# Kernel tuning notes

Hardware: AMD Instinct MI355X
Metric: run time of the kernel (lower is better)

## Reference

```python
import jax, jax.numpy as jnp
import numpy as np

HIDDEN = 32
INPUT = 1


def setup_inputs() -> dict:
    key = jax.random.key(0)
    ks = jax.random.split(key, 8)
    B, T = 4096, 512
    s = 1.0 / np.sqrt(HIDDEN)
    return {
        "x": jax.random.normal(ks[0], (B, T, INPUT), dtype=jnp.float32),
        "h0": jnp.zeros((1, B, HIDDEN), dtype=jnp.float32),
        "W_ih": jax.random.uniform(ks[1], (HIDDEN, INPUT), jnp.float32, -s, s),
        "b_ih": jax.random.uniform(ks[2], (HIDDEN,), jnp.float32, -s, s),
        "W_hh": jax.random.uniform(ks[3], (HIDDEN, HIDDEN), jnp.float32, -s, s),
        "b_hh": jax.random.uniform(ks[4], (HIDDEN,), jnp.float32, -s, s),
        "W_out": jax.random.uniform(ks[5], (1, HIDDEN), jnp.float32, -s, s),
        "b_out": jax.random.uniform(ks[6], (1,), jnp.float32, -s, s),
    }


def reference(x, h0, W_ih, b_ih, W_hh, b_hh, W_out, b_out):
    # Precompute input projection for all timesteps: [B, T, H]
    xp = jnp.einsum("bti,hi->bth", x, W_ih) + b_ih

    def step(h, xt):  # h: [B,H], xt: [B,H]
        h_new = jnp.tanh(xt + h @ W_hh.T + b_hh)
        return h_new, h_new

    hT, r_out = jax.lax.scan(step, h0[0], jnp.swapaxes(xp, 0, 1))  # r_out: [T,B,H]
    r_out = jnp.swapaxes(r_out, 0, 1)  # [B,T,H]
    # Per-timestep Linear(32->1) fused into one batched matmul
    outs = jnp.einsum("bth,oh->bto", r_out, W_out) + b_out  # [B,T,1]
    return outs, hT[None]  # h_state: [1,B,H]
```

## Files before the change

### kernel.cpp

```cpp
#include <hip/hip_runtime.h>

#define BATCH 4096
#define SEQT  512
#define HID   32

typedef _Float16 f16;
typedef _Float16 h2 __attribute__((ext_vector_type(2)));

#if __has_builtin(__builtin_amdgcn_fdot2)
#define FDOT2(a, b, c) __builtin_amdgcn_fdot2((a), (b), (c), false)
#else
#define FDOT2(a, b, c) fmaf((float)(a)[1], (float)(b)[1], fmaf((float)(a)[0], (float)(b)[0], (c)))
#endif

#if __has_builtin(__builtin_amdgcn_exp2f)
#define FAST_EXP2(x) __builtin_amdgcn_exp2f(x)
#else
#define FAST_EXP2(x) exp2f(x)
#endif
#if __has_builtin(__builtin_amdgcn_rcpf)
#define FAST_RCP(x) __builtin_amdgcn_rcpf(x)
#else
#define FAST_RCP(x) (1.0f / (x))
#endif

#define DPP_X1  0xB1
#define DPP_X2  0x4E
#define DPP_X7  0x141
#define DPP_X15 0x140

#if __has_builtin(__builtin_amdgcn_update_dpp)
template <int C, typename T>
__device__ __forceinline__ T xl(T v) {
    return __builtin_bit_cast(T, __builtin_amdgcn_update_dpp(
        0, __builtin_bit_cast(int, v), C, 0xF, 0xF, false));
}
#else
template <int C, typename T>
__device__ __forceinline__ T xl(T v) {
    constexpr int m = (C == DPP_X1) ? 1 : (C == DPP_X2) ? 2 : (C == DPP_X7) ? 7 : 15;
    return __builtin_bit_cast(T, __shfl_xor(__builtin_bit_cast(int, v), m));
}
#endif

__global__ __launch_bounds__(256) void rnn_kernel(
    const float* __restrict__ x,
    const float* __restrict__ h0,
    const float* __restrict__ W_ih,
    const float* __restrict__ b_ih,
    const float* __restrict__ W_hh,
    const float* __restrict__ b_hh,
    const float* __restrict__ W_out,
    const float* __restrict__ b_out,
    float* __restrict__ out)
{
    const int tid  = threadIdx.x;
    const int ell  = tid & 15;
    const int bseq = (blockIdx.x * 256 + tid) >> 4;
    const int j0 = 2 * ell, j1 = 2 * ell + 1;

    constexpr int MTBL[16] = {0, 1, 2, 3, 7, 6, 5, 4, 15, 14, 13, 12, 8, 9, 10, 11};

    h2 W0[16], W1[16];
    #pragma unroll
    for (int r = 0; r < 16; ++r) {
        const int p = ell ^ MTBL[r];
        const float2 w0 = *reinterpret_cast<const float2*>(W_hh + j0 * HID + 2 * p);
        const float2 w1 = *reinterpret_cast<const float2*>(W_hh + j1 * HID + 2 * p);
        W0[r] = h2{(f16)w0.x, (f16)w0.y};
        W1[r] = h2{(f16)w1.x, (f16)w1.y};
    }
    const float2 wo = *reinterpret_cast<const float2*>(W_out + j0);
    const h2 Wo2 = h2{(f16)wo.x, (f16)wo.y};
    const float wih0 = W_ih[j0], wih1 = W_ih[j1];
    const float bia0 = b_ih[j0] + b_hh[j0];
    const float bia1 = b_ih[j1] + b_hh[j1];
    const float bout = b_out[0];

    const float2 h0v = *reinterpret_cast<const float2*>(h0 + (size_t)bseq * HID + j0);
    h2 hcur = h2{(f16)h0v.x, (f16)h0v.y};
    float hn0 = h0v.x, hn1 = h0v.y;

    const float* xg = x + (size_t)bseq * SEQT;
    float*       og = out + (size_t)bseq * SEQT;

#define STEP(T2, XC) do {                                                     \
    h2 v0 = hcur;                                                             \
    h2 v1 = xl<DPP_X1>(v0);                                                   \
    h2 v2 = xl<DPP_X2>(v0);                                                   \
    h2 v3 = xl<DPP_X2>(v1);                                                   \
    h2 v4 = xl<DPP_X7>(v0);                                                   \
    h2 v5 = xl<DPP_X7>(v1);                                                   \
    h2 v6 = xl<DPP_X7>(v2);                                                   \
    h2 v7 = xl<DPP_X7>(v3);                                                   \
    h2 v8  = xl<DPP_X15>(v0);                                                 \
    h2 v9  = xl<DPP_X15>(v1);                                                 \
    h2 v10 = xl<DPP_X15>(v2);                                                 \
    h2 v11 = xl<DPP_X15>(v3);                                                 \
    h2 v12 = xl<DPP_X15>(v4);                                                 \
    h2 v13 = xl<DPP_X15>(v5);                                                 \
    h2 v14 = xl<DPP_X15>(v6);                                                 \
    h2 v15 = xl<DPP_X15>(v7);                                                 \
    float a0 = fmaf((XC), wih0, bia0);                                        \
    float b0 = fmaf((XC), wih1, bia1);                                        \
    a0 = FDOT2(v0,  W0[0],  a0);                                              \
    float a1 = FDOT2(v1,  W0[1],  0.0f);                                      \
    float a2 = FDOT2(v2,  W0[2],  0.0f);                                      \
    float a3 = FDOT2(v3,  W0[3],  0.0f);                                      \
    a0 = FDOT2(v4,  W0[4],  a0); a1 = FDOT2(v5,  W0[5],  a1);                 \
    a2 = FDOT2(v6,  W0[6],  a2); a3 = FDOT2(v7,  W0[7],  a3);                 \
    a0 = FDOT2(v8,  W0[8],  a0); a1 = FDOT2(v9,  W0[9],  a1);                 \
    a2 = FDOT2(v10, W0[10], a2); a3 = FDOT2(v11, W0[11], a3);                 \
    a0 = FDOT2(v12, W0[12], a0); a1 = FDOT2(v13, W0[13], a1);                 \
    a2 = FDOT2(v14, W0[14], a2); a3 = FDOT2(v15, W0[15], a3);                 \
    b0 = FDOT2(v0,  W1[0],  b0);                                              \
    float b1 = FDOT2(v1,  W1[1],  0.0f);                                      \
    float b2 = FDOT2(v2,  W1[2],  0.0f);                                      \
    float b3 = FDOT2(v3,  W1[3],  0.0f);                                      \
    b0 = FDOT2(v4,  W1[4],  b0); b1 = FDOT2(v5,  W1[5],  b1);                 \
    b2 = FDOT2(v6,  W1[6],  b2); b3 = FDOT2(v7,  W1[7],  b3);                 \
    b0 = FDOT2(v8,  W1[8],  b0); b1 = FDOT2(v9,  W1[9],  b1);                 \
    b2 = FDOT2(v10, W1[10], b2); b3 = FDOT2(v11, W1[11], b3);                 \
    b0 = FDOT2(v12, W1[12], b0); b1 = FDOT2(v13, W1[13], b1);                 \
    b2 = FDOT2(v14, W1[14], b2); b3 = FDOT2(v15, W1[15], b3);                 \
    const float s0 = (a0 + a1) + (a2 + a3);                                   \
    const float s1 = (b0 + b1) + (b2 + b3);                                   \
    const float e0 = FAST_EXP2(s0 * 2.8853900817779268f);                     \
    const float e1 = FAST_EXP2(s1 * 2.8853900817779268f);                     \
    hn0 = fmaf(-2.0f, FAST_RCP(e0 + 1.0f), 1.0f);                             \
    hn1 = fmaf(-2.0f, FAST_RCP(e1 + 1.0f), 1.0f);                             \
    hcur = h2{(f16)hn0, (f16)hn1};                                            \
    float pp = FDOT2(hcur, Wo2, 0.0f);                                        \
    pp += xl<DPP_X1>(pp);                                                     \
    pp += xl<DPP_X2>(pp);                                                     \
    pp += xl<DPP_X7>(pp);                                                     \
    pp += xl<DPP_X15>(pp);                                                    \
    if (ell == (T2)) osel = pp;                                               \
} while (0)

#define HALF(HC, Q0, Q1, Q2, Q3) do {                                         \
    float osel = 0.0f;                                                        \
    STEP(0,  (Q0).x); STEP(1,  (Q0).y); STEP(2,  (Q0).z); STEP(3,  (Q0).w);   \
    STEP(4,  (Q1).x); STEP(5,  (Q1).y); STEP(6,  (Q1).z); STEP(7,  (Q1).w);   \
    STEP(8,  (Q2).x); STEP(9,  (Q2).y); STEP(10, (Q2).z); STEP(11, (Q2).w);   \
    STEP(12, (Q3).x); STEP(13, (Q3).y); STEP(14, (Q3).z); STEP(15, (Q3).w);   \
    og[(HC) * 16 + ell] = osel + bout;                                        \
} while (0)

    const float4* xq0 = reinterpret_cast<const float4*>(xg);
    float4 qA0 = xq0[0], qA1 = xq0[1], qA2 = xq0[2], qA3 = xq0[3];
    float4 qB0, qB1, qB2, qB3;

    #pragma unroll 1
    for (int hc = 0; hc < 32; hc += 2) {
        const float4* pB = reinterpret_cast<const float4*>(xg + (hc + 1) * 16);
        qB0 = pB[0]; qB1 = pB[1]; qB2 = pB[2]; qB3 = pB[3];
        HALF(hc, qA0, qA1, qA2, qA3);
        const int tn = (hc + 2 < 32) ? (hc + 2) : 0;
        const float4* pA = reinterpret_cast<const float4*>(xg + tn * 16);
        qA0 = pA[0]; qA1 = pA[1]; qA2 = pA[2]; qA3 = pA[3];
        HALF(hc + 1, qB0, qB1, qB2, qB3);
    }

    float2 ht; ht.x = hn0; ht.y = hn1;
    *reinterpret_cast<float2*>(out + (size_t)BATCH * SEQT + (size_t)bseq * HID + j0) = ht;

#undef HALF
#undef STEP
}

extern "C" void kernel_launch(void* const* d_in, const int* in_sizes, int n_in,
                              void* d_out, int out_size, void* d_ws, size_t ws_size,
                              hipStream_t stream) {
    const float* x     = (const float*)d_in[0];
    const float* h0    = (const float*)d_in[1];
    const float* W_ih  = (const float*)d_in[2];
    const float* b_ih  = (const float*)d_in[3];
    const float* W_hh  = (const float*)d_in[4];
    const float* b_hh  = (const float*)d_in[5];
    const float* W_out = (const float*)d_in[6];
    const float* b_out = (const float*)d_in[7];
    float* outp = (float*)d_out;

    dim3 grid(BATCH * 16 / 256);
    dim3 block(256);
    hipLaunchKernelGGL(rnn_kernel, grid, block, 0, stream,
                       x, h0, W_ih, b_ih, W_hh, b_hh, W_out, b_out, outp);
}
```

Before: 168.6 us.

## Switch recurrence to fp32 packed FMA and batch output projection via LDS

Replaces the fp16 fdot2 recurrence with fp32 packed-FMA arithmetic on float2 vectors, which doubles the DPP lane exchanges per step (two 32-bit moves per shuffle). The per-step Linear(32->1) output reduction through DPP is removed. Instead, hidden states for 16 steps are staged in shared memory and each lane computes one output with a dot product after a wave barrier. This takes the output projection off the serial critical path, at the cost of more shuffles, more registers and LDS traffic. The higher precision also improves accuracy.

```diff
diff --git a/kernel.cpp b/kernel.cpp
--- a/kernel.cpp
+++ b/kernel.cpp
@@ -3,15 +3,12 @@
 #define BATCH 4096
 #define SEQT  512
 #define HID   32
-
-typedef _Float16 f16;
-typedef _Float16 h2 __attribute__((ext_vector_type(2)));
-
-#if __has_builtin(__builtin_amdgcn_fdot2)
-#define FDOT2(a, b, c) __builtin_amdgcn_fdot2((a), (b), (c), false)
-#else
-#define FDOT2(a, b, c) fmaf((float)(a)[1], (float)(b)[1], fmaf((float)(a)[0], (float)(b)[0], (c)))
-#endif
+#define WPB   4
+#define ROWF  36
+
+typedef float f32x2 __attribute__((ext_vector_type(2)));
+
+#define FMA2(a, b, c) __builtin_elementwise_fma((a), (b), (c))
 
 #if __has_builtin(__builtin_amdgcn_exp2f)
 #define FAST_EXP2(x) __builtin_amdgcn_exp2f(x)
@@ -29,21 +26,27 @@
 #define DPP_X7  0x141
 #define DPP_X15 0x140
 
-#if __has_builtin(__builtin_amdgcn_update_dpp)
-template <int C, typename T>
-__device__ __forceinline__ T xl(T v) {
-    return __builtin_bit_cast(T, __builtin_amdgcn_update_dpp(
-        0, __builtin_bit_cast(int, v), C, 0xF, 0xF, false));
+#if __has_builtin(__builtin_amdgcn_mov_dpp)
+#define XLI(x, C) __builtin_amdgcn_mov_dpp((x), (C), 0xF, 0xF, false)
+#elif __has_builtin(__builtin_amdgcn_update_dpp)
+#define XLI(x, C) __builtin_amdgcn_update_dpp(0, (x), (C), 0xF, 0xF, false)
+#else
+#define XLI(x, C) __shfl_xor((x), ((C) == DPP_X1) ? 1 : ((C) == DPP_X2) ? 2 : ((C) == DPP_X7) ? 7 : 15)
+#endif
+
+template <int C>
+__device__ __forceinline__ f32x2 xl2(f32x2 v) {
+    union { f32x2 f; int i[2]; } u, r;
+    u.f = v;
+    r.i[0] = XLI(u.i[0], C);
+    r.i[1] = XLI(u.i[1], C);
+    return r.f;
 }
-#else
-template <int C, typename T>
-__device__ __forceinline__ T xl(T v) {
-    constexpr int m = (C == DPP_X1) ? 1 : (C == DPP_X2) ? 2 : (C == DPP_X7) ? 7 : 15;
-    return __builtin_bit_cast(T, __shfl_xor(__builtin_bit_cast(int, v), m));
-}
-#endif
-
-__global__ __launch_bounds__(256) void rnn_kernel(
+
+__device__ __forceinline__ f32x2 lo2(float4 q) { f32x2 r; r.x = q.x; r.y = q.y; return r; }
+__device__ __forceinline__ f32x2 hi2(float4 q) { f32x2 r; r.x = q.z; r.y = q.w; return r; }
+
+__global__ __launch_bounds__(64 * WPB, 1) void rnn_kernel(
     const float* __restrict__ x,
     const float* __restrict__ h0,
     const float* __restrict__ W_ih,
@@ -55,96 +58,117 @@
     float* __restrict__ out)
 {
     const int tid  = threadIdx.x;
-    const int ell  = tid & 15;
-    const int bseq = (blockIdx.x * 256 + tid) >> 4;
+    const int wv   = tid >> 6;
+    const int lane = tid & 63;
+    const int g    = lane >> 4;
+    const int ell  = lane & 15;
+    const int bseq = blockIdx.x * (4 * WPB) + wv * 4 + g;
     const int j0 = 2 * ell, j1 = 2 * ell + 1;
 
+    __shared__ float hist_s[WPB][4][16][ROWF];
+
     constexpr int MTBL[16] = {0, 1, 2, 3, 7, 6, 5, 4, 15, 14, 13, 12, 8, 9, 10, 11};
 
-    h2 W0[16], W1[16];
+    f32x2 W0[16], W1[16];
     #pragma unroll
     for (int r = 0; r < 16; ++r) {
         const int p = ell ^ MTBL[r];
-        const float2 w0 = *reinterpret_cast<const float2*>(W_hh + j0 * HID + 2 * p);
-        const float2 w1 = *reinterpret_cast<const float2*>(W_hh + j1 * HID + 2 * p);
-        W0[r] = h2{(f16)w0.x, (f16)w0.y};
-        W1[r] = h2{(f16)w1.x, (f16)w1.y};
+        W0[r] = *reinterpret_cast<const f32x2*>(W_hh + j0 * HID + 2 * p);
+        W1[r] = *reinterpret_cast<const f32x2*>(W_hh + j1 * HID + 2 * p);
     }
-    const float2 wo = *reinterpret_cast<const float2*>(W_out + j0);
-    const h2 Wo2 = h2{(f16)wo.x, (f16)wo.y};
+    f32x2 Wo[16];
+    #pragma unroll
+    for (int r = 0; r < 16; ++r)
+        Wo[r] = *reinterpret_cast<const f32x2*>(W_out + 2 * r);
+
     const float wih0 = W_ih[j0], wih1 = W_ih[j1];
     const float bia0 = b_ih[j0] + b_hh[j0];
     const float bia1 = b_ih[j1] + b_hh[j1];
     const float bout = b_out[0];
-
-    const float2 h0v = *reinterpret_cast<const float2*>(h0 + (size_t)bseq * HID + j0);
-    h2 hcur = h2{(f16)h0v.x, (f16)h0v.y};
-    float hn0 = h0v.x, hn1 = h0v.y;
+    const f32x2 Z2 = {0.0f, 0.0f};
+
+    f32x2 hcur = *reinterpret_cast<const f32x2*>(h0 + (size_t)bseq * HID + j0);
 
     const float* xg = x + (size_t)bseq * SEQT;
     float*       og = out + (size_t)bseq * SEQT;
+    float*       hlane = &hist_s[wv][g][0][2 * ell];
 
 #define STEP(T2, XC) do {                                                     \
-    h2 v0 = hcur;                                                             \
-    h2 v1 = xl<DPP_X1>(v0);                                                   \
-    h2 v2 = xl<DPP_X2>(v0);                                                   \
-    h2 v3 = xl<DPP_X2>(v1);                                                   \
-    h2 v4 = xl<DPP_X7>(v0);                                                   \
-    h2 v5 = xl<DPP_X7>(v1);                                                   \
-    h2 v6 = xl<DPP_X7>(v2);                                                   \
-    h2 v7 = xl<DPP_X7>(v3);                                                   \
-    h2 v8  = xl<DPP_X15>(v0);                                                 \
-    h2 v9  = xl<DPP_X15>(v1);                                                 \
-    h2 v10 = xl<DPP_X15>(v2);                                                 \
-    h2 v11 = xl<DPP_X15>(v3);                                                 \
-    h2 v12 = xl<DPP_X15>(v4);                                                 \
-    h2 v13 = xl<DPP_X15>(v5);                                                 \
-    h2 v14 = xl<DPP_X15>(v6);                                                 \
-    h2 v15 = xl<DPP_X15>(v7);                                                 \
-    float a0 = fmaf((XC), wih0, bia0);                                        \
-    float b0 = fmaf((XC), wih1, bia1);                                        \
-    a0 = FDOT2(v0,  W0[0],  a0);                                              \
-    float a1 = FDOT2(v1,  W0[1],  0.0f);                                      \
-    float a2 = FDOT2(v2,  W0[2],  0.0f);                                      \
-    float a3 = FDOT2(v3,  W0[3],  0.0f);                                      \
-    a0 = FDOT2(v4,  W0[4],  a0); a1 = FDOT2(v5,  W0[5],  a1);                 \
-    a2 = FDOT2(v6,  W0[6],  a2); a3 = FDOT2(v7,  W0[7],  a3);                 \
-    a0 = FDOT2(v8,  W0[8],  a0); a1 = FDOT2(v9,  W0[9],  a1);                 \
-    a2 = FDOT2(v10, W0[10], a2); a3 = FDOT2(v11, W0[11], a3);                 \
-    a0 = FDOT2(v12, W0[12], a0); a1 = FDOT2(v13, W0[13], a1);                 \
-    a2 = FDOT2(v14, W0[14], a2); a3 = FDOT2(v15, W0[15], a3);                 \
-    b0 = FDOT2(v0,  W1[0],  b0);                                              \
-    float b1 = FDOT2(v1,  W1[1],  0.0f);                                      \
-    float b2 = FDOT2(v2,  W1[2],  0.0f);                                      \
-    float b3 = FDOT2(v3,  W1[3],  0.0f);                                      \
-    b0 = FDOT2(v4,  W1[4],  b0); b1 = FDOT2(v5,  W1[5],  b1);                 \
-    b2 = FDOT2(v6,  W1[6],  b2); b3 = FDOT2(v7,  W1[7],  b3);                 \
-    b0 = FDOT2(v8,  W1[8],  b0); b1 = FDOT2(v9,  W1[9],  b1);                 \
-    b2 = FDOT2(v10, W1[10], b2); b3 = FDOT2(v11, W1[11], b3);                 \
-    b0 = FDOT2(v12, W1[12], b0); b1 = FDOT2(v13, W1[13], b1);                 \
-    b2 = FDOT2(v14, W1[14], b2); b3 = FDOT2(v15, W1[15], b3);                 \
-    const float s0 = (a0 + a1) + (a2 + a3);                                   \
-    const float s1 = (b0 + b1) + (b2 + b3);                                   \
+    f32x2 v0 = hcur;                                                          \
+    f32x2 v1 = xl2<DPP_X1>(v0);                                               \
+    f32x2 v2 = xl2<DPP_X2>(v0);                                               \
+    f32x2 v3 = xl2<DPP_X2>(v1);                                               \
+    f32x2 v4 = xl2<DPP_X7>(v0);                                               \
+    f32x2 v5 = xl2<DPP_X7>(v1);                                               \
+    f32x2 v6 = xl2<DPP_X7>(v2);                                               \
+    f32x2 v7 = xl2<DPP_X7>(v3);                                               \
+    f32x2 v8  = xl2<DPP_X15>(v0);                                             \
+    f32x2 v9  = xl2<DPP_X15>(v1);                                             \
+    f32x2 v10 = xl2<DPP_X15>(v2);                                             \
+    f32x2 v11 = xl2<DPP_X15>(v3);                                             \
+    f32x2 v12 = xl2<DPP_X15>(v4);                                             \
+    f32x2 v13 = xl2<DPP_X15>(v5);                                             \
+    f32x2 v14 = xl2<DPP_X15>(v6);                                             \
+    f32x2 v15 = xl2<DPP_X15>(v7);                                             \
+    f32x2 A0; A0.x = fmaf((XC), wih0, bia0); A0.y = 0.0f;                     \
+    f32x2 B0; B0.x = fmaf((XC), wih1, bia1); B0.y = 0.0f;                     \
+    A0 = FMA2(v0, W0[0], A0);                                                 \
+    f32x2 A1 = FMA2(v1, W0[1], Z2);                                           \
+    f32x2 A2 = FMA2(v2, W0[2], Z2);                                           \
+    f32x2 A3 = FMA2(v3, W0[3], Z2);                                           \
+    A0 = FMA2(v4,  W0[4],  A0); A1 = FMA2(v5,  W0[5],  A1);                   \
+    A2 = FMA2(v6,  W0[6],  A2); A3 = FMA2(v7,  W0[7],  A3);                   \
+    A0 = FMA2(v8,  W0[8],  A0); A1 = FMA2(v9,  W0[9],  A1);                   \
+    A2 = FMA2(v10, W0[10], A2); A3 = FMA2(v11, W0[11], A3);                   \
+    A0 = FMA2(v12, W0[12], A0); A1 = FMA2(v13, W0[13], A1);                   \
+    A2 = FMA2(v14, W0[14], A2); A3 = FMA2(v15, W0[15], A3);                   \
+    B0 = FMA2(v0, W1[0], B0);                                                 \
+    f32x2 B1 = FMA2(v1, W1[1], Z2);                                           \
+    f32x2 B2 = FMA2(v2, W1[2], Z2);                                           \
+    f32x2 B3 = FMA2(v3, W1[3], Z2);                                           \
+    B0 = FMA2(v4,  W1[4],  B0); B1 = FMA2(v5,  W1[5],  B1);                   \
+    B2 = FMA2(v6,  W1[6],  B2); B3 = FMA2(v7,  W1[7],  B3);                   \
+    B0 = FMA2(v8,  W1[8],  B0); B1 = FMA2(v9,  W1[9],  B1);                   \
+    B2 = FMA2(v10, W1[10], B2); B3 = FMA2(v11, W1[11], B3);                   \
+    B0 = FMA2(v12, W1[12], B0); B1 = FMA2(v13, W1[13], B1);                   \
+    B2 = FMA2(v14, W1[14], B2); B3 = FMA2(v15, W1[15], B3);                   \
+    const f32x2 As = (A0 + A1) + (A2 + A3);                                   \
+    const f32x2 Bs = (B0 + B1) + (B2 + B3);                                   \
+    const float s0 = As.x + As.y;                                             \
+    const float s1 = Bs.x + Bs.y;                                             \
     const float e0 = FAST_EXP2(s0 * 2.8853900817779268f);                     \
     const float e1 = FAST_EXP2(s1 * 2.8853900817779268f);                     \
-    hn0 = fmaf(-2.0f, FAST_RCP(e0 + 1.0f), 1.0f);                             \
-    hn1 = fmaf(-2.0f, FAST_RCP(e1 + 1.0f), 1.0f);                             \
-    hcur = h2{(f16)hn0, (f16)hn1};                                            \
-    float pp = FDOT2(hcur, Wo2, 0.0f);                                        \
-    pp += xl<DPP_X1>(pp);                                                     \
-    pp += xl<DPP_X2>(pp);                                                     \
-    pp += xl<DPP_X7>(pp);                                                     \
-    pp += xl<DPP_X15>(pp);                                                    \
-    if (ell == (T2)) osel = pp;                                               \
+    f32x2 hc2;                                                                \
+    hc2.x = fmaf(-2.0f, FAST_RCP(e0 + 1.0f), 1.0f);                           \
+    hc2.y = fmaf(-2.0f, FAST_RCP(e1 + 1.0f), 1.0f);                           \
+    hcur = hc2;                                                               \
+    *reinterpret_cast<f32x2*>(hlane + (T2) * ROWF) = hcur;                    \
 } while (0)
 
 #define HALF(HC, Q0, Q1, Q2, Q3) do {                                         \
-    float osel = 0.0f;                                                        \
     STEP(0,  (Q0).x); STEP(1,  (Q0).y); STEP(2,  (Q0).z); STEP(3,  (Q0).w);   \
     STEP(4,  (Q1).x); STEP(5,  (Q1).y); STEP(6,  (Q1).z); STEP(7,  (Q1).w);   \
     STEP(8,  (Q2).x); STEP(9,  (Q2).y); STEP(10, (Q2).z); STEP(11, (Q2).w);   \
     STEP(12, (Q3).x); STEP(13, (Q3).y); STEP(14, (Q3).z); STEP(15, (Q3).w);   \
-    og[(HC) * 16 + ell] = osel + bout;                                        \
+    __builtin_amdgcn_wave_barrier();                                          \
+    {         \
+        const float4* rp = reinterpret_cast<const float4*>(&hist_s[wv][g][ell][0]); \
+        const float4 q0 = rp[0], q1 = rp[1], q2 = rp[2], q3 = rp[3];          \
+        const float4 q4 = rp[4], q5 = rp[5], q6 = rp[6], q7 = rp[7];          \
+        f32x2 o0 = FMA2(lo2(q0), Wo[0],  Z2);                                 \
+        f32x2 o1 = FMA2(hi2(q0), Wo[1],  Z2);                                 \
+        f32x2 o2 = FMA2(lo2(q1), Wo[2],  Z2);                                 \
+        f32x2 o3 = FMA2(hi2(q1), Wo[3],  Z2);                                 \
+        o0 = FMA2(lo2(q2), Wo[4],  o0); o1 = FMA2(hi2(q2), Wo[5],  o1);       \
+        o2 = FMA2(lo2(q3), Wo[6],  o2); o3 = FMA2(hi2(q3), Wo[7],  o3);       \
+        o0 = FMA2(lo2(q4), Wo[8],  o0); o1 = FMA2(hi2(q4), Wo[9],  o1);       \
+        o2 = FMA2(lo2(q5), Wo[10], o2); o3 = FMA2(hi2(q5), Wo[11], o3);       \
+        o0 = FMA2(lo2(q6), Wo[12], o0); o1 = FMA2(hi2(q6), Wo[13], o1);       \
+        o2 = FMA2(lo2(q7), Wo[14], o2); o3 = FMA2(hi2(q7), Wo[15], o3);       \
+        const f32x2 os = (o0 + o1) + (o2 + o3);                               \
+        og[(HC) * 16 + ell] = os.x + os.y + bout;                             \
+    }                                                                         \
+    __builtin_amdgcn_wave_barrier();                                          \
 } while (0)
 
     const float4* xq0 = reinterpret_cast<const float4*>(xg);
@@ -162,8 +186,7 @@
         HALF(hc + 1, qB0, qB1, qB2, qB3);
     }
 
-    float2 ht; ht.x = hn0; ht.y = hn1;
-    *reinterpret_cast<float2*>(out + (size_t)BATCH * SEQT + (size_t)bseq * HID + j0) = ht;
+    *reinterpret_cast<f32x2*>(out + (size_t)BATCH * SEQT + (size_t)bseq * HID + j0) = hcur;
 
 #undef HALF
 #undef STEP
@@ -182,8 +205,8 @@
     const float* b_out = (const float*)d_in[7];
     float* outp = (float*)d_out;
 
-    dim3 grid(BATCH * 16 / 256);
-    dim3 block(256);
+    dim3 grid(BATCH / (4 * WPB));
+    dim3 block(64 * WPB);
     hipLaunchKernelGGL(rnn_kernel, grid, block, 0, stream,
                        x, h0, W_ih, b_ih, W_hh, b_hh, W_out, b_out, outp);
 }
```

New measurement: 166.3 us. Within noise of the previous version (-1.3%).

## Compute RNN recurrence with MFMA 16x16x16 across 16 sequences per wave

Applied to the files above, without the earlier changes.

Replaces the per-lane fdot2 plus DPP-shuffle recurrence, where 16 lanes handle one sequence, with MFMA matrix ops: each 64-lane wave advances 16 sequences at once by multiplying the 32x32 W_hh (pre-scaled for exp2) against an f16 hidden-state matrix. The aim is to cut the per-step ALU and cross-lane traffic on the serial critical path. In exchange each step now carries MFMA latency, two ds_bpermute reductions for the output projection, and the launch drops to 256 single-wave blocks, which may underfill the GPU.

```diff
diff --git a/kernel.cpp b/kernel.cpp
--- a/kernel.cpp
+++ b/kernel.cpp
@@ -5,13 +5,10 @@
 #define HID   32
 
 typedef _Float16 f16;
-typedef _Float16 h2 __attribute__((ext_vector_type(2)));
+typedef _Float16 f16x4 __attribute__((ext_vector_type(4)));
+typedef float    f32x4 __attribute__((ext_vector_type(4)));
 
-#if __has_builtin(__builtin_amdgcn_fdot2)
-#define FDOT2(a, b, c) __builtin_amdgcn_fdot2((a), (b), (c), false)
-#else
-#define FDOT2(a, b, c) fmaf((float)(a)[1], (float)(b)[1], fmaf((float)(a)[0], (float)(b)[0], (c)))
-#endif
+#define MFMA16(a, b, c) __builtin_amdgcn_mfma_f32_16x16x16f16((a), (b), (c), 0, 0, 0)
 
 #if __has_builtin(__builtin_amdgcn_exp2f)
 #define FAST_EXP2(x) __builtin_amdgcn_exp2f(x)
@@ -24,26 +21,10 @@
 #define FAST_RCP(x) (1.0f / (x))
 #endif
 
-#define DPP_X1  0xB1
-#define DPP_X2  0x4E
-#define DPP_X7  0x141
-#define DPP_X15 0x140
+#define BCI(f) __builtin_bit_cast(int, (f))
+#define BCF(i) __builtin_bit_cast(float, (i))
 
-#if __has_builtin(__builtin_amdgcn_update_dpp)
-template <int C, typename T>
-__device__ __forceinline__ T xl(T v) {
-    return __builtin_bit_cast(T, __builtin_amdgcn_update_dpp(
-        0, __builtin_bit_cast(int, v), C, 0xF, 0xF, false));
-}
-#else
-template <int C, typename T>
-__device__ __forceinline__ T xl(T v) {
-    constexpr int m = (C == DPP_X1) ? 1 : (C == DPP_X2) ? 2 : (C == DPP_X7) ? 7 : 15;
-    return __builtin_bit_cast(T, __shfl_xor(__builtin_bit_cast(int, v), m));
-}
-#endif
-
-__global__ __launch_bounds__(256) void rnn_kernel(
+__global__ __launch_bounds__(64, 1) void rnn_kernel(
     const float* __restrict__ x,
     const float* __restrict__ h0,
     const float* __restrict__ W_ih,
@@ -54,118 +35,126 @@
     const float* __restrict__ b_out,
     float* __restrict__ out)
 {
-    const int tid  = threadIdx.x;
-    const int ell  = tid & 15;
-    const int bseq = (blockIdx.x * 256 + tid) >> 4;
-    const int j0 = 2 * ell, j1 = 2 * ell + 1;
+    const int lane = threadIdx.x & 63;
+    const int c    = lane & 15;
+    const int q    = lane >> 4;
+    const int seq  = blockIdx.x * 16 + c;
 
-    constexpr int MTBL[16] = {0, 1, 2, 3, 7, 6, 5, 4, 15, 14, 13, 12, 8, 9, 10, 11};
+    const float SC = 2.8853900817779268f;
 
-    h2 W0[16], W1[16];
+    f16x4 A00, A01, A10, A11;
+    {
+        const float4 w00 = *reinterpret_cast<const float4*>(W_hh + c * HID + 4 * q);
+        const float4 w01 = *reinterpret_cast<const float4*>(W_hh + c * HID + 16 + 4 * q);
+        const float4 w10 = *reinterpret_cast<const float4*>(W_hh + (16 + c) * HID + 4 * q);
+        const float4 w11 = *reinterpret_cast<const float4*>(W_hh + (16 + c) * HID + 16 + 4 * q);
+        A00 = f16x4{(f16)(SC * w00.x), (f16)(SC * w00.y), (f16)(SC * w00.z), (f16)(SC * w00.w)};
+        A01 = f16x4{(f16)(SC * w01.x), (f16)(SC * w01.y), (f16)(SC * w01.z), (f16)(SC * w01.w)};
+        A10 = f16x4{(f16)(SC * w10.x), (f16)(SC * w10.y), (f16)(SC * w10.z), (f16)(SC * w10.w)};
+        A11 = f16x4{(f16)(SC * w11.x), (f16)(SC * w11.y), (f16)(SC * w11.z), (f16)(SC * w11.w)};
+    }
+
+    float wihs[8], biass[8], wos[8];
     #pragma unroll
-    for (int r = 0; r < 16; ++r) {
-        const int p = ell ^ MTBL[r];
-        const float2 w0 = *reinterpret_cast<const float2*>(W_hh + j0 * HID + 2 * p);
-        const float2 w1 = *reinterpret_cast<const float2*>(W_hh + j1 * HID + 2 * p);
-        W0[r] = h2{(f16)w0.x, (f16)w0.y};
-        W1[r] = h2{(f16)w1.x, (f16)w1.y};
-    }
-    const float2 wo = *reinterpret_cast<const float2*>(W_out + j0);
-    const h2 Wo2 = h2{(f16)wo.x, (f16)wo.y};
-    const float wih0 = W_ih[j0], wih1 = W_ih[j1];
-    const float bia0 = b_ih[j0] + b_hh[j0];
-    const float bia1 = b_ih[j1] + b_hh[j1];
+    for (int m = 0; m < 2; ++m)
+        #pragma unroll
+        for (int r = 0; r < 4; ++r) {
+            const int h = 16 * m + 4 * q + r;
+            wihs[m * 4 + r]  = SC * W_ih[h];
+            biass[m * 4 + r] = SC * (b_ih[h] + b_hh[h]);
+            wos[m * 4 + r]   = W_out[h];
+        }
     const float bout = b_out[0];
 
-    const float2 h0v = *reinterpret_cast<const float2*>(h0 + (size_t)bseq * HID + j0);
-    h2 hcur = h2{(f16)h0v.x, (f16)h0v.y};
-    float hn0 = h0v.x, hn1 = h0v.y;
+    f16x4 Blo, Bhi;
+    {
+        const float4 lo = *reinterpret_cast<const float4*>(h0 + (size_t)seq * HID + 4 * q);
+        const float4 hi = *reinterpret_cast<const float4*>(h0 + (size_t)seq * HID + 16 + 4 * q);
+        Blo = f16x4{(f16)lo.x, (f16)lo.y, (f16)lo.z, (f16)lo.w};
+        Bhi = f16x4{(f16)hi.x, (f16)hi.y, (f16)hi.z, (f16)hi.w};
+    }
 
-    const float* xg = x + (size_t)bseq * SEQT;
-    float*       og = out + (size_t)bseq * SEQT;
+    const float* xg = x + (size_t)seq * SEQT;
+    float*       og = out + (size_t)seq * SEQT;
+
+    const int ix16 = (lane ^ 16) << 2;
+    const int ix32 = (lane ^ 32) << 2;
+
+    float hn[8];
+    float os[16];
 
 #define STEP(T2, XC) do {                                                     \
-    h2 v0 = hcur;                                                             \
-    h2 v1 = xl<DPP_X1>(v0);                                                   \
-    h2 v2 = xl<DPP_X2>(v0);                                                   \
-    h2 v3 = xl<DPP_X2>(v1);                                                   \
-    h2 v4 = xl<DPP_X7>(v0);                                                   \
-    h2 v5 = xl<DPP_X7>(v1);                                                   \
-    h2 v6 = xl<DPP_X7>(v2);                                                   \
-    h2 v7 = xl<DPP_X7>(v3);                                                   \
-    h2 v8  = xl<DPP_X15>(v0);                                                 \
-    h2 v9  = xl<DPP_X15>(v1);                                                 \
-    h2 v10 = xl<DPP_X15>(v2);                                                 \
-    h2 v11 = xl<DPP_X15>(v3);                                                 \
-    h2 v12 = xl<DPP_X15>(v4);                                                 \
-    h2 v13 = xl<DPP_X15>(v5);                                                 \
-    h2 v14 = xl<DPP_X15>(v6);                                                 \
-    h2 v15 = xl<DPP_X15>(v7);                                                 \
-    float a0 = fmaf((XC), wih0, bia0);                                        \
-    float b0 = fmaf((XC), wih1, bia1);                                        \
-    a0 = FDOT2(v0,  W0[0],  a0);                                              \
-    float a1 = FDOT2(v1,  W0[1],  0.0f);                                      \
-    float a2 = FDOT2(v2,  W0[2],  0.0f);                                      \
-    float a3 = FDOT2(v3,  W0[3],  0.0f);                                      \
-    a0 = FDOT2(v4,  W0[4],  a0); a1 = FDOT2(v5,  W0[5],  a1);                 \
-    a2 = FDOT2(v6,  W0[6],  a2); a3 = FDOT2(v7,  W0[7],  a3);                 \
-    a0 = FDOT2(v8,  W0[8],  a0); a1 = FDOT2(v9,  W0[9],  a1);                 \
-    a2 = FDOT2(v10, W0[10], a2); a3 = FDOT2(v11, W0[11], a3);                 \
-    a0 = FDOT2(v12, W0[12], a0); a1 = FDOT2(v13, W0[13], a1);                 \
-    a2 = FDOT2(v14, W0[14], a2); a3 = FDOT2(v15, W0[15], a3);                 \
-    b0 = FDOT2(v0,  W1[0],  b0);                                              \
-    float b1 = FDOT2(v1,  W1[1],  0.0f);                                      \
-    float b2 = FDOT2(v2,  W1[2],  0.0f);                                      \
-    float b3 = FDOT2(v3,  W1[3],  0.0f);                                      \
-    b0 = FDOT2(v4,  W1[4],  b0); b1 = FDOT2(v5,  W1[5],  b1);                 \
-    b2 = FDOT2(v6,  W1[6],  b2); b3 = FDOT2(v7,  W1[7],  b3);                 \
-    b0 = FDOT2(v8,  W1[8],  b0); b1 = FDOT2(v9,  W1[9],  b1);                 \
-    b2 = FDOT2(v10, W1[10], b2); b3 = FDOT2(v11, W1[11], b3);                 \
-    b0 = FDOT2(v12, W1[12], b0); b1 = FDOT2(v13, W1[13], b1);                 \
-    b2 = FDOT2(v14, W1[14], b2); b3 = FDOT2(v15, W1[15], b3);                 \
-    const float s0 = (a0 + a1) + (a2 + a3);                                   \
-    const float s1 = (b0 + b1) + (b2 + b3);                                   \
-    const float e0 = FAST_EXP2(s0 * 2.8853900817779268f);                     \
-    const float e1 = FAST_EXP2(s1 * 2.8853900817779268f);                     \
-    hn0 = fmaf(-2.0f, FAST_RCP(e0 + 1.0f), 1.0f);                             \
-    hn1 = fmaf(-2.0f, FAST_RCP(e1 + 1.0f), 1.0f);                             \
-    hcur = h2{(f16)hn0, (f16)hn1};                                            \
-    float pp = FDOT2(hcur, Wo2, 0.0f);                                        \
-    pp += xl<DPP_X1>(pp);                                                     \
-    pp += xl<DPP_X2>(pp);                                                     \
-    pp += xl<DPP_X7>(pp);                                                     \
-    pp += xl<DPP_X15>(pp);                                                    \
-    if (ell == (T2)) osel = pp;                                               \
+    f32x4 C0, C1;                                                             \
+    C0[0] = fmaf((XC), wihs[0], biass[0]);                                    \
+    C0[1] = fmaf((XC), wihs[1], biass[1]);                                    \
+    C0[2] = fmaf((XC), wihs[2], biass[2]);                                    \
+    C0[3] = fmaf((XC), wihs[3], biass[3]);                                    \
+    C1[0] = fmaf((XC), wihs[4], biass[4]);                                    \
+    C1[1] = fmaf((XC), wihs[5], biass[5]);                                    \
+    C1[2] = fmaf((XC), wihs[6], biass[6]);                                    \
+    C1[3] = fmaf((XC), wihs[7], biass[7]);                                    \
+    f32x4 D0 = MFMA16(A00, Blo, C0);                                          \
+    f32x4 D1 = MFMA16(A10, Blo, C1);                                          \
+    D0 = MFMA16(A01, Bhi, D0);                                                \
+    D1 = MFMA16(A11, Bhi, D1);                                                \
+    float o = 0.0f;                                                           \
+    _Pragma("unroll")                                                         \
+    for (int r = 0; r < 4; ++r) {                                             \
+        const float e0 = FAST_EXP2(D0[r]);                                    \
+        hn[r] = fmaf(-2.0f, FAST_RCP(e0 + 1.0f), 1.0f);                       \
+        const float e1 = FAST_EXP2(D1[r]);                                    \
+        hn[4 + r] = fmaf(-2.0f, FAST_RCP(e1 + 1.0f), 1.0f);                   \
+        o = fmaf(hn[r], wos[r], fmaf(hn[4 + r], wos[4 + r], o));              \
+    }                                                                         \
+    Blo = f16x4{(f16)hn[0], (f16)hn[1], (f16)hn[2], (f16)hn[3]};              \
+    Bhi = f16x4{(f16)hn[4], (f16)hn[5], (f16)hn[6], (f16)hn[7]};              \
+    o += BCF(__builtin_amdgcn_ds_bpermute(ix16, BCI(o)));                     \
+    o += BCF(__builtin_amdgcn_ds_bpermute(ix32, BCI(o)));                     \
+    os[T2] = o;                                                               \
 } while (0)
 
-#define HALF(HC, Q0, Q1, Q2, Q3) do {                                         \
-    float osel = 0.0f;                                                        \
+#define CHUNK(HC, Q0, Q1, Q2, Q3) do {                                        \
     STEP(0,  (Q0).x); STEP(1,  (Q0).y); STEP(2,  (Q0).z); STEP(3,  (Q0).w);   \
     STEP(4,  (Q1).x); STEP(5,  (Q1).y); STEP(6,  (Q1).z); STEP(7,  (Q1).w);   \
     STEP(8,  (Q2).x); STEP(9,  (Q2).y); STEP(10, (Q2).z); STEP(11, (Q2).w);   \
     STEP(12, (Q3).x); STEP(13, (Q3).y); STEP(14, (Q3).z); STEP(15, (Q3).w);   \
-    og[(HC) * 16 + ell] = osel + bout;                                        \
+    if (q == 0) {                                                             \
+        float4 s0, s1, s2, s3;                                                \
+        s0.x = os[0]  + bout; s0.y = os[1]  + bout;                           \
+        s0.z = os[2]  + bout; s0.w = os[3]  + bout;                           \
+        s1.x = os[4]  + bout; s1.y = os[5]  + bout;                           \
+        s1.z = os[6]  + bout; s1.w = os[7]  + bout;                           \
+        s2.x = os[8]  + bout; s2.y = os[9]  + bout;                           \
+        s2.z = os[10] + bout; s2.w = os[11] + bout;                           \
+        s3.x = os[12] + bout; s3.y = os[13] + bout;                           \
+        s3.z = os[14] + bout; s3.w = os[15] + bout;                           \
+        float4* op = reinterpret_cast<float4*>(og + (HC) * 16);               \
+        op[0] = s0; op[1] = s1; op[2] = s2; op[3] = s3;                       \
+    }                                                                         \
 } while (0)
 
-    const float4* xq0 = reinterpret_cast<const float4*>(xg);
-    float4 qA0 = xq0[0], qA1 = xq0[1], qA2 = xq0[2], qA3 = xq0[3];
-    float4 qB0, qB1, qB2, qB3;
+    const float4* xp0 = reinterpret_cast<const float4*>(xg);
+    float4 a0 = xp0[0], a1 = xp0[1], a2 = xp0[2], a3 = xp0[3];
+    float4 b0, b1, b2, b3;
 
     #pragma unroll 1
     for (int hc = 0; hc < 32; hc += 2) {
         const float4* pB = reinterpret_cast<const float4*>(xg + (hc + 1) * 16);
-        qB0 = pB[0]; qB1 = pB[1]; qB2 = pB[2]; qB3 = pB[3];
-        HALF(hc, qA0, qA1, qA2, qA3);
+        b0 = pB[0]; b1 = pB[1]; b2 = pB[2]; b3 = pB[3];
+        CHUNK(hc, a0, a1, a2, a3);
         const int tn = (hc + 2 < 32) ? (hc + 2) : 0;
         const float4* pA = reinterpret_cast<const float4*>(xg + tn * 16);
-        qA0 = pA[0]; qA1 = pA[1]; qA2 = pA[2]; qA3 = pA[3];
-        HALF(hc + 1, qB0, qB1, qB2, qB3);
+        a0 = pA[0]; a1 = pA[1]; a2 = pA[2]; a3 = pA[3];
+        CHUNK(hc + 1, b0, b1, b2, b3);
     }
 
-    float2 ht; ht.x = hn0; ht.y = hn1;
-    *reinterpret_cast<float2*>(out + (size_t)BATCH * SEQT + (size_t)bseq * HID + j0) = ht;
+    float* hp = out + (size_t)BATCH * SEQT + (size_t)seq * HID;
+    float4 t0; t0.x = hn[0]; t0.y = hn[1]; t0.z = hn[2]; t0.w = hn[3];
+    float4 t1; t1.x = hn[4]; t1.y = hn[5]; t1.z = hn[6]; t1.w = hn[7];
+    *reinterpret_cast<float4*>(hp + 4 * q)      = t0;
+    *reinterpret_cast<float4*>(hp + 16 + 4 * q) = t1;
 
-#undef HALF
+#undef CHUNK
 #undef STEP
 }
 
@@ -182,8 +171,8 @@
     const float* b_out = (const float*)d_in[7];
     float* outp = (float*)d_out;
 
-    dim3 grid(BATCH * 16 / 256);
-    dim3 block(256);
+    dim3 grid(BATCH / 16);
+    dim3 block(64);
     hipLaunchKernelGGL(rnn_kernel, grid, block, 0, stream,
                        x, h0, W_ih, b_ih, W_hh, b_hh, W_out, b_out, outp);
 }
```

Measured after the change: 176.5 us. +4.7%, slower.
